# Performance work log

Measured on AMD Instinct MI355X. Metric: run time of the kernel, lower is better.

The kernel has to match this reference:

```python
import jax, jax.numpy as jnp
from jax import lax
import numpy as np

NUM_HEADS = 8
KW = 3  # window kernel size

def _avgpool3(x):
    # x: [B,C,H,W]; AvgPool2d(3,1,1) with count_include_pad=True -> sum/9
    s = lax.reduce_window(x, 0.0, lax.add, (1, 1, KW, KW), (1, 1, 1, 1),
                          ((0, 0), (0, 0), (1, 1), (1, 1)))
    return s / (KW * KW)

def _unfold3(y):
    # y: [B,h,w,C] -> [B,h,w,9,C]; patch index ordered row-major (kh,kw)
    B, h, w, C = y.shape
    yp = jnp.pad(y, ((0, 0), (1, 1), (1, 1), (0, 0)))
    return jnp.stack([yp[:, i:i + h, j:j + w, :]
                      for i in range(KW) for j in range(KW)], axis=3)

def setup_inputs():
    key = jax.random.key(0)
    ks = jax.random.split(key, 9)
    B, C, H, W = 8, 256, 64, 64
    sd = 0.02
    return {
        "x": jax.random.normal(ks[0], (B, C, H, W), jnp.float32),
        "W_qkv": jax.random.normal(ks[1], (4 * C, C), jnp.float32) * sd,
        "b_qkv": jnp.zeros((4 * C,), jnp.float32),
        "W1": jax.random.normal(ks[2], (C // 2, C), jnp.float32) * sd,
        "b1": jnp.zeros((C // 2,), jnp.float32),
        "W2": jax.random.normal(ks[3], (C, C // 2), jnp.float32) * sd,
        "b2": jnp.zeros((C,), jnp.float32),
        "Wp": jax.random.normal(ks[4], (C, C), jnp.float32) * sd,
        "bp": jnp.zeros((C,), jnp.float32),
    }

def reference(x, W_qkv, b_qkv, W1, b1, W2, b2, Wp, bp):
    B, C, H, W = x.shape
    nH = NUM_HEADS
    hd = C // nH
    scale = hd ** -0.5
    # avg pool (stride 1 keeps spatial dims), to channels-last
    y = _avgpool3(x).transpose(0, 2, 3, 1)                 # [B,h,w,C]
    qkv = y @ W_qkv.T + b_qkv                              # [B,h,w,4C]
    qkv = qkv.reshape(B, H, W, C, 4)
    q, k, v, chans = qkv[..., 0], qkv[..., 1], qkv[..., 2], qkv[..., 3]
    # channel gate
    g = jax.nn.sigmoid(jax.nn.relu(chans @ W1.T + b1) @ W2.T + b2)  # [B,h,w,C]
    # local window attention: each query attends to its 3x3 neighborhood
    qh = q.reshape(B, H, W, nH, hd)                        # [B,h,w,n,d]
    kp = _unfold3(k).reshape(B, H, W, KW * KW, nH, hd)     # [B,h,w,9,n,d]
    vp = _unfold3(v).reshape(B, H, W, KW * KW, nH, hd)
    attn = jnp.einsum('bhwnd,bhwknd->bhwnk', qh, kp) * scale
    attn = jax.nn.softmax(attn, axis=-1)
    out = jnp.einsum('bhwnk,bhwknd->bhwnd', attn, vp).reshape(B, H, W, C)
    out = out * g + out
    out = out @ Wp.T + bp
    return out.transpose(0, 3, 1, 2)                       # [B,C,H,W]
```

## Files before the change

kernel.cpp:

```cpp
#include <hip/hip_runtime.h>
#include <stdint.h>

typedef __bf16    bf16x8 __attribute__((ext_vector_type(8)));
typedef float     f32x4  __attribute__((ext_vector_type(4)));
typedef uint32_t  u32x4  __attribute__((ext_vector_type(4)));

#define MFMA(a,b,c) __builtin_amdgcn_mfma_f32_16x16x32_bf16((a),(b),(c),0,0,0)

__device__ __align__(16) uint16_t g_y [8*64*64*256];
__device__ __align__(16) uint16_t g_wpk[393216];

#define WQF 0
#define WKF 65536
#define WVF 131072
#define WCF 196608
#define W1F 262144
#define W2F 294912
#define WPF 327680

static __device__ __forceinline__ float b2f(uint32_t u){ return __builtin_bit_cast(float, u<<16); }
static __device__ __forceinline__ float b2fh(uint32_t u){ return __builtin_bit_cast(float, u & 0xffff0000u); }
static __device__ __forceinline__ uint32_t f2b(float f){
  uint32_t x = __builtin_bit_cast(uint32_t, f);
  return (x + 0x7fffu + ((x>>16)&1u)) >> 16;
}

__global__ __launch_bounds__(256) void kpack(const float* __restrict__ Wqkv,
    const float* __restrict__ W1, const float* __restrict__ W2,
    const float* __restrict__ Wp){
  int idx = blockIdx.x*256 + threadIdx.x;
  int j = idx & 7, lane = (idx>>3)&63;
  int n16 = lane & 15, q4 = lane>>4;
  float v;
  if (idx < 262144){
    int t = idx >> 16, l = idx & 65535;
    int s = (l>>9)&7, nt = l>>12;
    v = Wqkv[(4*(nt*16+n16) + t)*256 + s*32 + q4*8 + j];
  } else if (idx < 294912){
    int l = idx - 262144;
    int s = (l>>9)&7, nt = l>>12;
    v = W1[(nt*16+n16)*256 + s*32 + q4*8 + j];
  } else if (idx < 327680){
    int l = idx - 294912;
    int s = (l>>9)&3, nt = l>>11;
    v = W2[(nt*16+n16)*128 + s*32 + q4*8 + j];
  } else {
    int l = idx - 327680;
    int s = (l>>9)&7, nt = l>>12;
    v = Wp[(nt*16+n16)*256 + s*32 + q4*8 + j];
  }
  g_wpk[idx] = (uint16_t)f2b(v);
}

__global__ __launch_bounds__(512) void kpool(const float* __restrict__ x){
  __shared__ __align__(16) uint16_t sm[3*256*82];
  uint32_t* smw = (uint32_t*)sm;
  int t = threadIdx.x;
  int b = blockIdx.x >> 6, h = blockIdx.x & 63;
  for (int i=t; i<768; i+=512){
    int base = i*41;
    smw[base+3]  = 0;
    smw[base+36] = 0;
  }
  if (h==0 || h==63){
    int hh = (h==0) ? 0 : 2;
    for (int i=t; i<10496; i+=512) smw[hh*10496 + i] = 0;
  }
  #pragma unroll
  for (int i=0;i<24;i++){
    int id = t + 512*i;
    int w4 = id&15, c = (id>>4)&255, hh = id>>12;
    int gy = h - 1 + hh;
    if ((unsigned)gy < 64u){
      f32x4 ld = *(const f32x4*)&x[(((b*256+c)*64+gy)*64) + w4*4];
      int wb = (((hh*256+c)*82 + 8 + w4*4) >> 1);
      smw[wb+0] = f2b(ld[0]) | (f2b(ld[1])<<16);
      smw[wb+1] = f2b(ld[2]) | (f2b(ld[3])<<16);
    }
  }
  __syncthreads();
  int c = t & 255, wsel = t >> 8;
  int r0 = c*82, r1 = r0 + 256*82, r2 = r1 + 256*82;
  int w0 = wsel*32;
  float csp = b2f(sm[r0+w0+7]) + b2f(sm[r1+w0+7]) + b2f(sm[r2+w0+7]);
  float csc = b2f(sm[r0+w0+8]) + b2f(sm[r1+w0+8]) + b2f(sm[r2+w0+8]);
  uint16_t* dst = g_y + ((b*64+h)*64)*256 + c;
  for (int j2=0;j2<32;j2++){
    int w = w0 + j2;
    float csn = b2f(sm[r0+w+9]) + b2f(sm[r1+w+9]) + b2f(sm[r2+w+9]);
    float yv = (csp + csc + csn) * (1.0f/9.0f);
    dst[w*256] = (uint16_t)f2b(yv);
    csp = csc; csc = csn;
  }
}

#define YSTR 264
#define HSTR 136
#define YS 0
#define QS 26400
#define KS 35104
#define VS 48704
#define MCH 0
#define MHS 16896
#define MAO 26400
__global__ __launch_bounds__(1024) void kattn(const float* __restrict__ bqkv,
    const float* __restrict__ b1, const float* __restrict__ b2v,
    const float* __restrict__ bp, float* __restrict__ out){
  __shared__ __align__(16) uint16_t sm[62304];
  int t = threadIdx.x;
  int lane = t & 63, wave = t >> 6;
  int n16 = lane & 15, quad = lane >> 4;
  int bid = blockIdx.x;
  int bb = bid>>6, tyhi=(bid>>4)&3, txl=(bid>>3)&1, tylo=(bid>>2)&1, txp=bid&3;
  int ty = tyhi*2+tylo, tx = txp*2+txl;

  uint32_t opk[2][8];
  uint32_t chp[16];

  #pragma unroll
  for (int i=0;i<4;i++){
    int id = t + 1024*i;
    if (id < 3200){
      int hp = id >> 5, c8 = id & 31;
      int py = hp/10, px = hp - py*10;
      int gy = ty*8 + py - 1, gx = tx*8 + px - 1;
      u32x4 ld = {0,0,0,0};
      if ((unsigned)gy<64u && (unsigned)gx<64u)
        ld = *(const u32x4*)&g_y[((bb*64+gy)*64+gx)*256 + c8*8];
      *(u32x4*)&sm[hp*YSTR + c8*8] = ld;
    }
  }
  __syncthreads();

  #pragma unroll
  for (int hf=0; hf<2; hf++){
    {
      int ntg = wave & 7;
      int ntgg = hf*8 + ntg;
      bool isK = wave < 8;
      int colB = ntg*16;
      {
        bf16x8 Bx[8];
        const uint16_t* wb = &g_wpk[(isK?WKF:WVF)];
        #pragma unroll
        for (int s=0;s<8;s++) Bx[s] = *(const bf16x8*)&wb[((ntgg*8+s)*64+lane)*8];
        float bx = bqkv[4*(ntgg*16+n16) + (isK?1:2)];
        int base = isK ? KS : VS;
        #pragma unroll
        for (int mt=0; mt<7; mt++){
          f32x4 a = {0.f,0.f,0.f,0.f};
          int m = mt*16 + n16;
          int mr = (m < 100) ? m : 99;
          #pragma unroll
          for (int s=0;s<8;s++){
            bf16x8 A = *(const bf16x8*)&sm[YS + mr*YSTR + s*32 + quad*8];
            a = MFMA(A, Bx[s], a);
          }
          #pragma unroll
          for (int r=0;r<4;r++){
            int row = mt*16 + quad*4 + r;
            if (row < 100){
              int py = row/10, px = row - py*10;
              int gy = ty*8 + py - 1, gx = tx*8 + px - 1;
              bool ok = ((unsigned)gy<64u) && ((unsigned)gx<64u);
              sm[base + row*HSTR + colB + n16] = (uint16_t)f2b(ok ? a[r]+bx : 0.f);
            }
          }
        }
      }
      {
        bf16x8 Bq[8];
        #pragma unroll
        for (int s=0;s<8;s++) Bq[s] = *(const bf16x8*)&g_wpk[WQF + ((ntgg*8+s)*64+lane)*8];
        float bq = bqkv[4*(ntgg*16+n16) + 0];
        int mt0 = isK ? 0 : 2;
        #pragma unroll
        for (int mi=0; mi<2; mi++){
          int mt = mt0 + mi;
          f32x4 a = {0.f,0.f,0.f,0.f};
          int m = mt*16 + n16;
          int hrow = 10*(m>>3) + (m&7) + 11;
          #pragma unroll
          for (int s=0;s<8;s++){
            bf16x8 A = *(const bf16x8*)&sm[YS + hrow*YSTR + s*32 + quad*8];
            a = MFMA(A, Bq[s], a);
          }
          #pragma unroll
          for (int r=0;r<4;r++){
            int row = mt*16 + quad*4 + r;
            sm[QS + row*HSTR + colB + n16] = (uint16_t)f2b(a[r] + bq);
          }
        }
      }
    }
    __syncthreads();
    if (wave < 8){
      int h = wave >> 1, ph = wave & 1;
      int pl = lane & 31, dh = lane >> 5;
      int p = ph*32 + pl;
      int iy = p >> 3, ix = p & 7;
      int co = h*32 + dh*16;
      u32x4 qa = *(const u32x4*)&sm[QS + p*HSTR + co];
      u32x4 qb = *(const u32x4*)&sm[QS + p*HSTR + co + 8];
      float qv[16];
      #pragma unroll
      for (int i=0;i<4;i++){
        qv[2*i]   = b2f(qa[i]);  qv[2*i+1]   = b2fh(qa[i]);
        qv[8+2*i] = b2f(qb[i]);  qv[8+2*i+1] = b2fh(qb[i]);
      }
      int hb = (iy+1)*10 + ix + 1;
      const int off[9] = {-11,-10,-9,-1,0,1,9,10,11};
      float sc[9];
      #pragma unroll
      for (int nb=0;nb<9;nb++){
        const uint16_t* kr = &sm[KS + (hb+off[nb])*HSTR + co];
        u32x4 ka = *(const u32x4*)kr;
        u32x4 kb = *(const u32x4*)(kr+8);
        float s = 0.f;
        #pragma unroll
        for (int i=0;i<4;i++){
          s += qv[2*i]*b2f(ka[i]) + qv[2*i+1]*b2fh(ka[i]);
          s += qv[8+2*i]*b2f(kb[i]) + qv[8+2*i+1]*b2fh(kb[i]);
        }
        sc[nb] = s;
      }
      #pragma unroll
      for (int nb=0;nb<9;nb++) sc[nb] = (sc[nb] + __shfl_xor(sc[nb], 32)) * 0.17677669529663687f;
      float mx = sc[0];
      #pragma unroll
      for (int nb=1;nb<9;nb++) mx = fmaxf(mx, sc[nb]);
      float l = 0.f;
      #pragma unroll
      for (int nb=0;nb<9;nb++){ sc[nb] = __expf(sc[nb]-mx); l += sc[nb]; }
      float inv = 1.f / l;
      float o[16];
      #pragma unroll
      for (int i=0;i<16;i++) o[i]=0.f;
      #pragma unroll
      for (int nb=0;nb<9;nb++){
        float wgt = sc[nb]*inv;
        const uint16_t* vr = &sm[VS + (hb+off[nb])*HSTR + co];
        u32x4 va = *(const u32x4*)vr;
        u32x4 vb = *(const u32x4*)(vr+8);
        #pragma unroll
        for (int i=0;i<4;i++){
          o[2*i]     += wgt*b2f(va[i]);  o[2*i+1]   += wgt*b2fh(va[i]);
          o[8+2*i]   += wgt*b2f(vb[i]);  o[8+2*i+1] += wgt*b2fh(vb[i]);
        }
      }
      #pragma unroll
      for (int i=0;i<8;i++) opk[hf][i] = f2b(o[2*i]) | (f2b(o[2*i+1])<<16);
    } else if (hf == 0){
      #pragma unroll
      for (int jj=0;jj<2;jj++){
        int ntg = (wave-8)*2 + jj;
        bf16x8 Bc[8];
        #pragma unroll
        for (int s=0;s<8;s++) Bc[s] = *(const bf16x8*)&g_wpk[WCF + ((ntg*8+s)*64+lane)*8];
        float bc = bqkv[4*(ntg*16+n16) + 3];
        #pragma unroll
        for (int mt=0; mt<4; mt++){
          f32x4 a = {0.f,0.f,0.f,0.f};
          int m = mt*16 + n16;
          int hrow = 10*(m>>3) + (m&7) + 11;
          #pragma unroll
          for (int s=0;s<8;s++){
            bf16x8 A = *(const bf16x8*)&sm[YS + hrow*YSTR + s*32 + quad*8];
            a = MFMA(A, Bc[s], a);
          }
          chp[(jj*4+mt)*2+0] = f2b(a[0]+bc) | (f2b(a[1]+bc)<<16);
          chp[(jj*4+mt)*2+1] = f2b(a[2]+bc) | (f2b(a[3]+bc)<<16);
        }
      }
    } else {
      #pragma unroll
      for (int jj=0;jj<2;jj++){
        int ntg = (wave-8)*2 + jj;
        int col = ntg*16 + n16;
        #pragma unroll
        for (int mt=0;mt<4;mt++){
          #pragma unroll
          for (int r2=0;r2<2;r2++){
            uint32_t v = chp[(jj*4+mt)*2+r2];
            int row = mt*16 + quad*4 + r2*2;
            sm[MCH + row*YSTR + col]        = (uint16_t)(v & 0xffffu);
            sm[MCH + (row+1)*YSTR + col]    = (uint16_t)(v >> 16);
          }
        }
      }
    }
    __syncthreads();
  }
  if (wave < 8){
    int h = wave >> 1, ph = wave & 1;
    int pl = lane & 31, dh = lane >> 5;
    int p = ph*32 + pl;
    int co = h*32 + dh*16;
    #pragma unroll
    for (int hf=0;hf<2;hf++){
      u32x4 s0 = {opk[hf][0],opk[hf][1],opk[hf][2],opk[hf][3]};
      u32x4 s1 = {opk[hf][4],opk[hf][5],opk[hf][6],opk[hf][7]};
      *(u32x4*)&sm[MAO + p*YSTR + hf*128 + co]     = s0;
      *(u32x4*)&sm[MAO + p*YSTR + hf*128 + co + 8] = s1;
    }
  } else {
    int ntg = wave - 8;
    bf16x8 Bf[8];
    #pragma unroll
    for (int s=0;s<8;s++) Bf[s] = *(const bf16x8*)&g_wpk[W1F + ((ntg*8+s)*64+lane)*8];
    float bs = b1[ntg*16+n16];
    int colB = ntg*16;
    #pragma unroll
    for (int mt=0;mt<4;mt++){
      f32x4 a = {0.f,0.f,0.f,0.f};
      #pragma unroll
      for (int s=0;s<8;s++){
        bf16x8 A = *(const bf16x8*)&sm[MCH + (mt*16+n16)*YSTR + s*32 + quad*8];
        a = MFMA(A, Bf[s], a);
      }
      #pragma unroll
      for (int r=0;r<4;r++){
        int row = mt*16 + quad*4 + r;
        sm[MHS + row*HSTR + colB + n16] = (uint16_t)f2b(fmaxf(a[r]+bs, 0.f));
      }
    }
  }
  __syncthreads();
  {
    int ntg = wave;
    bf16x8 Bf[4];
    #pragma unroll
    for (int s=0;s<4;s++) Bf[s] = *(const bf16x8*)&g_wpk[W2F + ((ntg*4+s)*64+lane)*8];
    float bs = b2v[ntg*16+n16];
    int colB = ntg*16;
    #pragma unroll
    for (int mt=0;mt<4;mt++){
      f32x4 a = {0.f,0.f,0.f,0.f};
      #pragma unroll
      for (int s=0;s<4;s++){
        bf16x8 A = *(const bf16x8*)&sm[MHS + (mt*16+n16)*HSTR + s*32 + quad*8];
        a = MFMA(A, Bf[s], a);
      }
      #pragma unroll
      for (int r=0;r<4;r++){
        int row = mt*16 + quad*4 + r;
        float gg = 1.f/(1.f+__expf(-(a[r] + bs)));
        float ao = b2f((uint32_t)sm[MAO + row*YSTR + colB + n16]);
        sm[MCH + row*YSTR + colB + n16] = (uint16_t)f2b(ao*(1.f+gg));
      }
    }
  }
  __syncthreads();
  {
    int ntg = wave;
    bf16x8 Bf[8];
    #pragma unroll
    for (int s=0;s<8;s++) Bf[s] = *(const bf16x8*)&g_wpk[WPF + ((ntg*8+s)*64+lane)*8];
    float bs = bp[ntg*16+n16];
    int colB = ntg*16;
    #pragma unroll
    for (int mt=0;mt<4;mt++){
      f32x4 a = {0.f,0.f,0.f,0.f};
      #pragma unroll
      for (int s=0;s<8;s++){
        bf16x8 A = *(const bf16x8*)&sm[MCH + (mt*16+n16)*YSTR + s*32 + quad*8];
        a = MFMA(A, Bf[s], a);
      }
      #pragma unroll
      for (int r=0;r<4;r++){
        int row = mt*16 + quad*4 + r;
        sm[MAO + row*YSTR + colB + n16] = (uint16_t)f2b(a[r]+bs);
      }
    }
  }
  __syncthreads();
  #pragma unroll
  for (int i=0;i<4;i++){
    int idx = t + 1024*i;
    int ix4 = idx&1, iy = (idx>>1)&7, c = idx>>4;
    f32x4 stv;
    #pragma unroll
    for (int j=0;j<4;j++){
      int p = iy*8 + ix4*4 + j;
      stv[j] = b2f((uint32_t)sm[MAO + p*YSTR + c]);
    }
    *(f32x4*)&out[(((bb*256+c)*64) + ty*8+iy)*64 + tx*8 + ix4*4] = stv;
  }
}

extern "C" void kernel_launch(void* const* d_in, const int* in_sizes, int n_in,
                              void* d_out, int out_size, void* d_ws, size_t ws_size,
                              hipStream_t stream){
  (void)in_sizes; (void)n_in; (void)d_ws; (void)ws_size; (void)out_size;
  const float* x    = (const float*)d_in[0];
  const float* Wqkv = (const float*)d_in[1];
  const float* bqkv = (const float*)d_in[2];
  const float* W1   = (const float*)d_in[3];
  const float* b1   = (const float*)d_in[4];
  const float* W2   = (const float*)d_in[5];
  const float* b2   = (const float*)d_in[6];
  const float* Wp   = (const float*)d_in[7];
  const float* bp   = (const float*)d_in[8];
  kpack<<<dim3(1536), dim3(256), 0, stream>>>(Wqkv, W1, W2, Wp);
  kpool<<<dim3(512),  dim3(512), 0, stream>>>(x);
  kattn<<<dim3(512),  dim3(1024), 0, stream>>>(bqkv, b1, b2, bp, (float*)d_out);
}
```

Measured before the change: 204.5 us.

## Write attention output directly to dedicated LDS buffer and split W1 GEMM across all waves

The attention output is now stored to a new dedicated shared-memory region (padded stride) as soon as each half is computed, instead of being held in registers across the loop and written out after the final barrier. This frees sixteen registers per thread and lets all 16 waves share the W1 gate GEMM, each doing two M-tiles instead of eight waves doing four. Shared memory grows to about 159 KB per block, which still fits one 1024-thread block per CU but leaves little headroom. The padded stride is intended to reduce LDS bank conflicts on the gate-multiply reads.

Result: slower. 211.1 us (+3.3%).

```diff
diff --git a/kernel.cpp b/kernel.cpp
--- a/kernel.cpp
+++ b/kernel.cpp
@@ -96,17 +96,19 @@
 
 #define YSTR 264
 #define HSTR 136
+#define AOSTR 268
 #define YS 0
 #define QS 26400
 #define KS 35104
 #define VS 48704
+#define AOB 62304
 #define MCH 0
 #define MHS 16896
 #define MAO 26400
 __global__ __launch_bounds__(1024) void kattn(const float* __restrict__ bqkv,
     const float* __restrict__ b1, const float* __restrict__ b2v,
     const float* __restrict__ bp, float* __restrict__ out){
-  __shared__ __align__(16) uint16_t sm[62304];
+  __shared__ __align__(16) uint16_t sm[79456];
   int t = threadIdx.x;
   int lane = t & 63, wave = t >> 6;
   int n16 = lane & 15, quad = lane >> 4;
@@ -114,7 +116,6 @@
   int bb = bid>>6, tyhi=(bid>>4)&3, txl=(bid>>3)&1, tylo=(bid>>2)&1, txp=bid&3;
   int ty = tyhi*2+tylo, tx = txp*2+txl;
 
-  uint32_t opk[2][8];
   uint32_t chp[16];
 
   #pragma unroll
@@ -141,9 +142,9 @@
       int colB = ntg*16;
       {
         bf16x8 Bx[8];
-        const uint16_t* wb = &g_wpk[(isK?WKF:WVF)];
-        #pragma unroll
-        for (int s=0;s<8;s++) Bx[s] = *(const bf16x8*)&wb[((ntgg*8+s)*64+lane)*8];
+        const uint16_t* wbase = &g_wpk[(isK?WKF:WVF)];
+        #pragma unroll
+        for (int s=0;s<8;s++) Bx[s] = *(const bf16x8*)&wbase[((ntgg*8+s)*64+lane)*8];
         float bx = bqkv[4*(ntgg*16+n16) + (isK?1:2)];
         int base = isK ? KS : VS;
         #pragma unroll
@@ -248,8 +249,15 @@
           o[8+2*i]   += wgt*b2f(vb[i]);  o[8+2*i+1] += wgt*b2fh(vb[i]);
         }
       }
-      #pragma unroll
-      for (int i=0;i<8;i++) opk[hf][i] = f2b(o[2*i]) | (f2b(o[2*i+1])<<16);
+      uint16_t* aop = &sm[AOB + p*AOSTR + hf*128 + co];
+      u32x4 s0, s1;
+      #pragma unroll
+      for (int i=0;i<4;i++){
+        s0[i] = f2b(o[2*i])   | (f2b(o[2*i+1])<<16);
+        s1[i] = f2b(o[8+2*i]) | (f2b(o[8+2*i+1])<<16);
+      }
+      *(u32x4*)&aop[0] = s0;
+      *(u32x4*)&aop[8] = s1;
     } else if (hf == 0){
       #pragma unroll
       for (int jj=0;jj<2;jj++){
@@ -291,27 +299,17 @@
     }
     __syncthreads();
   }
-  if (wave < 8){
-    int h = wave >> 1, ph = wave & 1;
-    int pl = lane & 31, dh = lane >> 5;
-    int p = ph*32 + pl;
-    int co = h*32 + dh*16;
-    #pragma unroll
-    for (int hf=0;hf<2;hf++){
-      u32x4 s0 = {opk[hf][0],opk[hf][1],opk[hf][2],opk[hf][3]};
-      u32x4 s1 = {opk[hf][4],opk[hf][5],opk[hf][6],opk[hf][7]};
-      *(u32x4*)&sm[MAO + p*YSTR + hf*128 + co]     = s0;
-      *(u32x4*)&sm[MAO + p*YSTR + hf*128 + co + 8] = s1;
-    }
-  } else {
-    int ntg = wave - 8;
+  {
+    int ntg = wave & 7;
+    int mt0 = (wave >> 3) * 2;
     bf16x8 Bf[8];
     #pragma unroll
     for (int s=0;s<8;s++) Bf[s] = *(const bf16x8*)&g_wpk[W1F + ((ntg*8+s)*64+lane)*8];
     float bs = b1[ntg*16+n16];
     int colB = ntg*16;
     #pragma unroll
-    for (int mt=0;mt<4;mt++){
+    for (int mi=0;mi<2;mi++){
+      int mt = mt0 + mi;
       f32x4 a = {0.f,0.f,0.f,0.f};
       #pragma unroll
       for (int s=0;s<8;s++){
@@ -345,7 +343,7 @@
       for (int r=0;r<4;r++){
         int row = mt*16 + quad*4 + r;
         float gg = 1.f/(1.f+__expf(-(a[r] + bs)));
-        float ao = b2f((uint32_t)sm[MAO + row*YSTR + colB + n16]);
+        float ao = b2f((uint32_t)sm[AOB + row*AOSTR + colB + n16]);
         sm[MCH + row*YSTR + colB + n16] = (uint16_t)f2b(ao*(1.f+gg));
       }
     }
```
